# Kernel optimization log

Measured on AMD Instinct MI355X. Metric: run time of the kernel, lower is better.

The kernel has to match this reference:

```python
import jax, jax.numpy as jnp
import numpy as np

N, Q, D = 16384, 16384, 3
RADIUS = 0.08  # ~30 expected neighbors for uniform points in [0,1]^3


def setup_inputs() -> dict:
    key = jax.random.key(0)
    k1, k2 = jax.random.split(key)
    data = jax.random.uniform(k1, (N, D), dtype=jnp.float32)
    queries = jax.random.uniform(k2, (Q, D), dtype=jnp.float32)
    return {"data": data, "queries": queries, "radius": RADIUS}


def reference(data, queries, radius):
    # Pairwise squared Euclidean distances [Q, N] via ||q||^2 + ||d||^2 - 2 q.d
    # (avoids materializing the [Q, N, D] difference tensor).
    q2 = jnp.sum(queries * queries, axis=-1)[:, None]   # [Q, 1]
    d2 = jnp.sum(data * data, axis=-1)[None, :]         # [1, N]
    sqdist = jnp.maximum(q2 + d2 - 2.0 * (queries @ data.T), 0.0)  # [Q, N]

    # Ball query: dist <= radius  <=>  sqdist <= radius^2 (sklearn query_radius semantics)
    mask = sqdist <= (radius * radius)                  # [Q, N] bool

    # Ragged row splits: [0, cumsum(per-query neighbor counts)] -> [Q+1]
    counts = jnp.sum(mask.astype(jnp.int32), axis=1)    # [Q]
    row_splits = jnp.concatenate(
        [jnp.zeros((1,), dtype=jnp.int32), jnp.cumsum(counts)]
    )

    # weights = squared distance for in-radius pairs (dense padded form of the
    # torch module's concatenated ragged 'weights' = dist**2)
    weights = jnp.where(mask, sqdist, jnp.float32(0.0))  # [Q, N]

    return mask, row_splits, weights
```

## Files before the change

### kernel.cpp

```cpp
#include <hip/hip_runtime.h>
#include <cstddef>


namespace {

constexpr int NPTS = 16384;
constexpr int NQ   = 16384;
constexpr int QB   = 8;
constexpr int TPB  = 256;
constexpr int VEC  = 8;
constexpr int ITERS = NPTS / (TPB * VEC);

__device__ __forceinline__ float mulrn(float a, float b) { return __fmul_rn(a, b); }
__device__ __forceinline__ float addrn(float a, float b) { return __fadd_rn(a, b); }

__device__ __forceinline__ float sqdist(float qx, float qy, float qz, float q2,
                                        float dx, float dy, float dz, float d2) {
    const float dot = __fmaf_rn(qx, dx, __fmaf_rn(qy, dy, __fmul_rn(qz, dz)));
    const float s   = __fmaf_rn(-2.0f, dot, __fadd_rn(q2, d2));
    return fmaxf(s, 0.0f);
}

__device__ __forceinline__ float norm2(float x, float y, float z) {
    return __fmaf_rn(x, x, __fmaf_rn(y, y, __fmul_rn(z, z)));
}

__global__ __launch_bounds__(TPB) void ball_kernel(
    const float* __restrict__ data,
    const float* __restrict__ queries,
    const float* __restrict__ radius_p,
    float* __restrict__ out,
    int* __restrict__ counts)
{
    const int tid  = threadIdx.x;
    const int lane = tid & 63;
    const int q0   = blockIdx.x * QB;

    __shared__ float qs[(QB + 1) * 3];
    __shared__ int   scnt[QB];
    if (tid < (QB + 1) * 3) {
        int src = q0 * 3 - 3 + tid;
        if (src < 0) src = 0;
        qs[tid] = queries[src];
    }
    if (tid < QB) scnt[tid] = 0;
    __syncthreads();

    const float r  = radius_p[0];
    const float r2 = mulrn(r, r);

    const float lxx = data[(size_t)(NPTS - 1) * 3 + 0];
    const float lyy = data[(size_t)(NPTS - 1) * 3 + 1];
    const float lzz = data[(size_t)(NPTS - 1) * 3 + 2];
    const float l2  = norm2(lxx, lyy, lzz);

    float qx[QB], qy[QB], qz[QB], q2v[QB], whead[QB];
#pragma unroll
    for (int i = 0; i < QB; ++i) {
        qx[i] = qs[3 * (i + 1) + 0];
        qy[i] = qs[3 * (i + 1) + 1];
        qz[i] = qs[3 * (i + 1) + 2];
        q2v[i] = norm2(qx[i], qy[i], qz[i]);
        const float px = qs[3 * i + 0], py = qs[3 * i + 1], pz = qs[3 * i + 2];
        const float p2 = norm2(px, py, pz);
        const float sq = sqdist(px, py, pz, p2, lxx, lyy, lzz, l2);
        whead[i] = (sq <= r2) ? sq : 0.0f;
    }

    int cnt[QB];
#pragma unroll
    for (int i = 0; i < QB; ++i) cnt[i] = 0;

    float* __restrict__ mask = out;
    float* __restrict__ wts  = out + ((size_t)NQ * NPTS + NQ + 1);

    for (int it = 0; it < ITERS; ++it) {
        const int nb = (it * TPB + tid) * VEC;
        const float* dbase = data + (size_t)nb * 3;
        const float4 dA = *reinterpret_cast<const float4*>(dbase + 0);
        const float4 dB = *reinterpret_cast<const float4*>(dbase + 4);
        const float4 dC = *reinterpret_cast<const float4*>(dbase + 8);
        const float4 dD = *reinterpret_cast<const float4*>(dbase + 12);
        const float4 dE = *reinterpret_cast<const float4*>(dbase + 16);
        const float4 dF = *reinterpret_cast<const float4*>(dbase + 20);
        const float dx[VEC] = {dA.x, dA.w, dB.z, dC.y, dD.x, dD.w, dE.z, dF.y};
        const float dy[VEC] = {dA.y, dB.x, dB.w, dC.z, dD.y, dE.x, dE.w, dF.z};
        const float dz[VEC] = {dA.z, dB.y, dC.x, dC.w, dD.z, dE.y, dF.x, dF.w};
        float d2[VEC];
#pragma unroll
        for (int j = 0; j < VEC; ++j) d2[j] = norm2(dx[j], dy[j], dz[j]);

        const int pm1 = (nb == 0) ? 0 : nb - 1;
        const float mx = data[(size_t)pm1 * 3 + 0];
        const float my = data[(size_t)pm1 * 3 + 1];
        const float mz = data[(size_t)pm1 * 3 + 2];
        const float m2 = norm2(mx, my, mz);

        const bool rowhead = (tid == 0 && it == 0);

#pragma unroll
        for (int q = 0; q < QB; ++q) {
            float m[VEC], w[VEC];
#pragma unroll
            for (int j = 0; j < VEC; ++j) {
                const float sq = sqdist(qx[q], qy[q], qz[q], q2v[q],
                                        dx[j], dy[j], dz[j], d2[j]);
                const bool in = (sq <= r2);
                m[j] = in ? 1.0f : 0.0f;
                w[j] = in ? sq : 0.0f;
                cnt[q] += in ? 1 : 0;
            }
            const float sqm = sqdist(qx[q], qy[q], qz[q], q2v[q], mx, my, mz, m2);
            const float wprev = (sqm <= r2) ? sqm : 0.0f;
            const float wsh = __shfl_up(w[7], 1);
            float slot0 = (lane == 0) ? wprev : wsh;
            if (rowhead) slot0 = whead[q];

            const size_t row = (size_t)(q0 + q) * NPTS;
            *reinterpret_cast<float4*>(mask + row + nb) =
                make_float4(m[0], m[1], m[2], m[3]);
            *reinterpret_cast<float4*>(mask + row + nb + 4) =
                make_float4(m[4], m[5], m[6], m[7]);
            *reinterpret_cast<float4*>(wts + row + nb - 1) =
                make_float4(slot0, w[0], w[1], w[2]);
            *reinterpret_cast<float4*>(wts + row + nb + 3) =
                make_float4(w[3], w[4], w[5], w[6]);
        }
    }

    if (q0 == NQ - QB && tid == TPB - 1) {
        const float sq = sqdist(qx[QB-1], qy[QB-1], qz[QB-1], q2v[QB-1],
                                lxx, lyy, lzz, l2);
        wts[(size_t)(NQ - 1) * NPTS + (NPTS - 1)] = (sq <= r2) ? sq : 0.0f;
    }

#pragma unroll
    for (int q = 0; q < QB; ++q) {
        int v = cnt[q];
        for (int off = 32; off >= 1; off >>= 1) v += __shfl_down(v, off);
        if ((tid & 63) == 0) atomicAdd(&scnt[q], v);
    }
    __syncthreads();
    if (tid < QB) counts[q0 + tid] = scnt[tid];
}

constexpr int STPB  = 256;
constexpr int CHUNK = NQ / STPB;

__global__ __launch_bounds__(STPB) void scan_kernel(
    const int* __restrict__ counts, float* __restrict__ out)
{
    __shared__ int sums[STPB];
    const int tid  = threadIdx.x;
    const int base = tid * CHUNK;

    int s = 0;
    for (int i = 0; i < CHUNK; ++i) s += counts[base + i];
    sums[tid] = s;
    __syncthreads();

    for (int off = 1; off < STPB; off <<= 1) {
        int v = 0;
        if (tid >= off) v = sums[tid - off];
        __syncthreads();
        sums[tid] += v;
        __syncthreads();
    }

    int run = (tid == 0) ? 0 : sums[tid - 1];
    float* rs = out + (size_t)NQ * NPTS;
    if (tid == 0) rs[0] = 0.0f;
    for (int i = 0; i < CHUNK; ++i) {
        run += counts[base + i];
        rs[base + i + 1] = (float)run;
    }
}

}

extern "C" void kernel_launch(void* const* d_in, const int* in_sizes, int n_in,
                              void* d_out, int out_size, void* d_ws, size_t ws_size,
                              hipStream_t stream) {
    const float* data    = (const float*)d_in[0];
    const float* queries = (const float*)d_in[1];
    const float* radius  = (const float*)d_in[2];
    float* out  = (float*)d_out;
    int* counts = (int*)d_ws;

    hipLaunchKernelGGL(ball_kernel, dim3(NQ / QB), dim3(TPB), 0, stream,
                       data, queries, radius, out, counts);
    hipLaunchKernelGGL(scan_kernel, dim3(1), dim3(STPB), 0, stream, counts, out);
}
```

Baseline: 442.4 us.

## Interchange query and data loops so each query row streams contiguously

Swaps the loop nest so the outer loop walks the 8 queries and the inner loop walks the data points. Each pass now writes one contiguous mask row and one weights row, and register pressure drops from holding 8 query states and counts. The cost is that data points are reloaded once per query (8x the data reads, mostly from cache), their norms are recomputed, and both loops are marked unroll 1, which cuts instruction-level parallelism. The count reduction moves inside the per-query loop.

After: 409.6 us. 1.08x faster.

```diff
diff --git a/kernel.cpp b/kernel.cpp
--- a/kernel.cpp
+++ b/kernel.cpp
@@ -11,18 +11,15 @@
 constexpr int VEC  = 8;
 constexpr int ITERS = NPTS / (TPB * VEC);
 
-__device__ __forceinline__ float mulrn(float a, float b) { return __fmul_rn(a, b); }
-__device__ __forceinline__ float addrn(float a, float b) { return __fadd_rn(a, b); }
+__device__ __forceinline__ float norm2(float x, float y, float z) {
+    return __fmaf_rn(x, x, __fmaf_rn(y, y, __fmul_rn(z, z)));
+}
 
 __device__ __forceinline__ float sqdist(float qx, float qy, float qz, float q2,
                                         float dx, float dy, float dz, float d2) {
     const float dot = __fmaf_rn(qx, dx, __fmaf_rn(qy, dy, __fmul_rn(qz, dz)));
     const float s   = __fmaf_rn(-2.0f, dot, __fadd_rn(q2, d2));
     return fmaxf(s, 0.0f);
-}
-
-__device__ __forceinline__ float norm2(float x, float y, float z) {
-    return __fmaf_rn(x, x, __fmaf_rn(y, y, __fmul_rn(z, z)));
 }
 
 __global__ __launch_bounds__(TPB) void ball_kernel(
@@ -47,99 +44,93 @@
     __syncthreads();
 
     const float r  = radius_p[0];
-    const float r2 = mulrn(r, r);
+    const float r2 = __fmul_rn(r, r);
 
     const float lxx = data[(size_t)(NPTS - 1) * 3 + 0];
     const float lyy = data[(size_t)(NPTS - 1) * 3 + 1];
     const float lzz = data[(size_t)(NPTS - 1) * 3 + 2];
     const float l2  = norm2(lxx, lyy, lzz);
 
-    float qx[QB], qy[QB], qz[QB], q2v[QB], whead[QB];
-#pragma unroll
-    for (int i = 0; i < QB; ++i) {
-        qx[i] = qs[3 * (i + 1) + 0];
-        qy[i] = qs[3 * (i + 1) + 1];
-        qz[i] = qs[3 * (i + 1) + 2];
-        q2v[i] = norm2(qx[i], qy[i], qz[i]);
-        const float px = qs[3 * i + 0], py = qs[3 * i + 1], pz = qs[3 * i + 2];
-        const float p2 = norm2(px, py, pz);
-        const float sq = sqdist(px, py, pz, p2, lxx, lyy, lzz, l2);
-        whead[i] = (sq <= r2) ? sq : 0.0f;
-    }
-
-    int cnt[QB];
-#pragma unroll
-    for (int i = 0; i < QB; ++i) cnt[i] = 0;
-
     float* __restrict__ mask = out;
     float* __restrict__ wts  = out + ((size_t)NQ * NPTS + NQ + 1);
 
-    for (int it = 0; it < ITERS; ++it) {
-        const int nb = (it * TPB + tid) * VEC;
-        const float* dbase = data + (size_t)nb * 3;
-        const float4 dA = *reinterpret_cast<const float4*>(dbase + 0);
-        const float4 dB = *reinterpret_cast<const float4*>(dbase + 4);
-        const float4 dC = *reinterpret_cast<const float4*>(dbase + 8);
-        const float4 dD = *reinterpret_cast<const float4*>(dbase + 12);
-        const float4 dE = *reinterpret_cast<const float4*>(dbase + 16);
-        const float4 dF = *reinterpret_cast<const float4*>(dbase + 20);
-        const float dx[VEC] = {dA.x, dA.w, dB.z, dC.y, dD.x, dD.w, dE.z, dF.y};
-        const float dy[VEC] = {dA.y, dB.x, dB.w, dC.z, dD.y, dE.x, dE.w, dF.z};
-        const float dz[VEC] = {dA.z, dB.y, dC.x, dC.w, dD.z, dE.y, dF.x, dF.w};
-        float d2[VEC];
-#pragma unroll
-        for (int j = 0; j < VEC; ++j) d2[j] = norm2(dx[j], dy[j], dz[j]);
+#pragma unroll 1
+    for (int q = 0; q < QB; ++q) {
+        const float qxq = qs[3 * (q + 1) + 0];
+        const float qyq = qs[3 * (q + 1) + 1];
+        const float qzq = qs[3 * (q + 1) + 2];
+        const float q2q = norm2(qxq, qyq, qzq);
 
-        const int pm1 = (nb == 0) ? 0 : nb - 1;
-        const float mx = data[(size_t)pm1 * 3 + 0];
-        const float my = data[(size_t)pm1 * 3 + 1];
-        const float mz = data[(size_t)pm1 * 3 + 2];
-        const float m2 = norm2(mx, my, mz);
+        const float px = qs[3 * q + 0], py = qs[3 * q + 1], pz = qs[3 * q + 2];
+        const float sqh = sqdist(px, py, pz, norm2(px, py, pz), lxx, lyy, lzz, l2);
+        const float wheadq = (sqh <= r2) ? sqh : 0.0f;
 
-        const bool rowhead = (tid == 0 && it == 0);
+        float* __restrict__ mrow = mask + (size_t)(q0 + q) * NPTS;
+        float* __restrict__ wrow = wts  + (size_t)(q0 + q) * NPTS;
 
-#pragma unroll
-        for (int q = 0; q < QB; ++q) {
+        int cnt = 0;
+
+#pragma unroll 1
+        for (int it = 0; it < ITERS; ++it) {
+            const int nb = (it * TPB + tid) * VEC;
+            const float* dbase = data + (size_t)nb * 3;
+            const float4 dA = *reinterpret_cast<const float4*>(dbase + 0);
+            const float4 dB = *reinterpret_cast<const float4*>(dbase + 4);
+            const float4 dC = *reinterpret_cast<const float4*>(dbase + 8);
+            const float4 dD = *reinterpret_cast<const float4*>(dbase + 12);
+            const float4 dE = *reinterpret_cast<const float4*>(dbase + 16);
+            const float4 dF = *reinterpret_cast<const float4*>(dbase + 20);
+
+            const int pm1 = (nb == 0) ? 0 : nb - 1;
+            const float mx = data[(size_t)pm1 * 3 + 0];
+            const float my = data[(size_t)pm1 * 3 + 1];
+            const float mz = data[(size_t)pm1 * 3 + 2];
+
+            const float dx[VEC] = {dA.x, dA.w, dB.z, dC.y, dD.x, dD.w, dE.z, dF.y};
+            const float dy[VEC] = {dA.y, dB.x, dB.w, dC.z, dD.y, dE.x, dE.w, dF.z};
+            const float dz[VEC] = {dA.z, dB.y, dC.x, dC.w, dD.z, dE.y, dF.x, dF.w};
+
             float m[VEC], w[VEC];
 #pragma unroll
             for (int j = 0; j < VEC; ++j) {
-                const float sq = sqdist(qx[q], qy[q], qz[q], q2v[q],
-                                        dx[j], dy[j], dz[j], d2[j]);
+                const float d2 = norm2(dx[j], dy[j], dz[j]);
+                const float sq = sqdist(qxq, qyq, qzq, q2q, dx[j], dy[j], dz[j], d2);
                 const bool in = (sq <= r2);
                 m[j] = in ? 1.0f : 0.0f;
                 w[j] = in ? sq : 0.0f;
-                cnt[q] += in ? 1 : 0;
+                cnt += in ? 1 : 0;
             }
-            const float sqm = sqdist(qx[q], qy[q], qz[q], q2v[q], mx, my, mz, m2);
+
+            const float m2  = norm2(mx, my, mz);
+            const float sqm = sqdist(qxq, qyq, qzq, q2q, mx, my, mz, m2);
             const float wprev = (sqm <= r2) ? sqm : 0.0f;
             const float wsh = __shfl_up(w[7], 1);
             float slot0 = (lane == 0) ? wprev : wsh;
-            if (rowhead) slot0 = whead[q];
+            if (tid == 0 && it == 0) slot0 = wheadq;
 
-            const size_t row = (size_t)(q0 + q) * NPTS;
-            *reinterpret_cast<float4*>(mask + row + nb) =
+            *reinterpret_cast<float4*>(mrow + nb) =
                 make_float4(m[0], m[1], m[2], m[3]);
-            *reinterpret_cast<float4*>(mask + row + nb + 4) =
+            *reinterpret_cast<float4*>(mrow + nb + 4) =
                 make_float4(m[4], m[5], m[6], m[7]);
-            *reinterpret_cast<float4*>(wts + row + nb - 1) =
+            *reinterpret_cast<float4*>(wrow + nb - 1) =
                 make_float4(slot0, w[0], w[1], w[2]);
-            *reinterpret_cast<float4*>(wts + row + nb + 3) =
+            *reinterpret_cast<float4*>(wrow + nb + 3) =
                 make_float4(w[3], w[4], w[5], w[6]);
         }
+
+        for (int off = 32; off >= 1; off >>= 1) cnt += __shfl_down(cnt, off);
+        if (lane == 0) atomicAdd(&scnt[q], cnt);
     }
 
     if (q0 == NQ - QB && tid == TPB - 1) {
-        const float sq = sqdist(qx[QB-1], qy[QB-1], qz[QB-1], q2v[QB-1],
+        const float qxq = qs[3 * QB + 0];
+        const float qyq = qs[3 * QB + 1];
+        const float qzq = qs[3 * QB + 2];
+        const float sq = sqdist(qxq, qyq, qzq, norm2(qxq, qyq, qzq),
                                 lxx, lyy, lzz, l2);
         wts[(size_t)(NQ - 1) * NPTS + (NPTS - 1)] = (sq <= r2) ? sq : 0.0f;
     }
 
-#pragma unroll
-    for (int q = 0; q < QB; ++q) {
-        int v = cnt[q];
-        for (int off = 32; off >= 1; off >>= 1) v += __shfl_down(v, off);
-        if ((tid & 63) == 0) atomicAdd(&scnt[q], v);
-    }
     __syncthreads();
     if (tid < QB) counts[q0 + tid] = scnt[tid];
 }
```
